# Kernel tuning notes

Measured on AMD Instinct MI355X. Metric: run time of the kernel, lower is better.

The kernel has to match this reference:

```python
import jax, jax.numpy as jnp
import numpy as np


def setup_inputs() -> dict:
    key = jax.random.key(0)
    ks = jax.random.split(key, 9)
    B, C, H, W = 4, 256, 128, 128
    d = C // 8
    x = jax.random.normal(ks[0], (B, C, H, W), jnp.float32)
    wq = jax.random.normal(ks[1], (d, C), jnp.float32) * 0.05
    bq = jax.random.normal(ks[2], (d,), jnp.float32) * 0.05
    wk = jax.random.normal(ks[3], (d, C), jnp.float32) * 0.05
    bk = jax.random.normal(ks[4], (d,), jnp.float32) * 0.05
    wv = jax.random.normal(ks[5], (d, C), jnp.float32) * 0.05
    bv = jax.random.normal(ks[6], (d,), jnp.float32) * 0.05
    wp = jax.random.normal(ks[7], (C, d, 3, 3), jnp.float32) * 0.05
    gamma = jax.random.normal(ks[8], (1,), jnp.float32)
    return dict(x=x, wq=wq, bq=bq, wk=wk, bk=bk, wv=wv, bv=bv, wp=wp, gamma=gamma)


def reference(x, wq, bq, wk, bk, wv, bv, wp, gamma):
    B, C, H, W = x.shape
    d = wq.shape[0]  # C // 8
    N = H * W
    # 1x1 convs expressed as channel matmuls
    q = jnp.einsum('bchw,dc->bdhw', x, wq) + bq[None, :, None, None]
    k = jnp.einsum('bchw,dc->bdhw', x, wk) + bk[None, :, None, None]
    v = jnp.einsum('bchw,dc->bdhw', x, wv) + bv[None, :, None, None]
    Q = q.reshape(B, d, N)
    K = k.reshape(B, d, N)
    V = v.reshape(B, d, N)
    # channel-channel energy: [B, d, d]
    energy = jnp.einsum('bdn,ben->bde', Q, K)
    energy_new = jnp.max(energy, axis=-1, keepdims=True) - energy
    attention = jax.nn.softmax(energy_new, axis=-1)
    out = jnp.einsum('bde,ben->bdn', attention, V).reshape(B, d, H, W)
    # 3x3 conv (no bias) + exact GELU
    out = jax.lax.conv_general_dilated(
        out, wp, window_strides=(1, 1), padding='SAME',
        dimension_numbers=('NCHW', 'OIHW', 'NCHW'))
    out = jax.nn.gelu(out, approximate=False)
    return gamma[0] * out + x
```

## Files before the change

### kernel.cpp

```cpp
#include <hip/hip_runtime.h>
#include <hip/hip_bf16.h>
#include <math.h>

#define BB 4
#define CC 256
#define HH 128
#define WW 128
#define NN (HH*WW)
#define DD 32

#define AOT_CI   44
#define AOT_ROWE (130*AOT_CI)
#define AOT_IMGE (130*AOT_ROWE)
#define AOT_BYTES ((size_t)BB*AOT_IMGE*2)
#define AOT_ALLOC (AOT_BYTES + 1024)

#define WT_BYTES (9*256*AOT_CI*2)

#define PATCH_SZ 45760
#define WSLAB    22528
#define CONV_LDS (PATCH_SZ + 2*WSLAB)
#define EPI_PITCH 260

#define ASWZ_BYTES 98304
#define QKP 260

typedef __attribute__((ext_vector_type(8)))  short bf16x8;
typedef __attribute__((ext_vector_type(4)))  float f32x4;
typedef __attribute__((ext_vector_type(16))) float f32x16;

__device__ inline void async_copy16(void* lds, const void* g) {
    __builtin_amdgcn_global_load_lds(
        (const __attribute__((address_space(1))) unsigned int*)g,
        (__attribute__((address_space(3))) unsigned int*)lds, 16, 0, 0);
}

__device__ inline unsigned short f2bf(float f) {
    __hip_bfloat16 h = __float2bfloat16(f);
    return *reinterpret_cast<unsigned short*>(&h);
}

__device__ inline void split2(float v, unsigned short& h, unsigned short& l) {
    __hip_bfloat16 hb = __float2bfloat16(v);
    float r = v - __bfloat162float(hb);
    __hip_bfloat16 lb = __float2bfloat16(r);
    h = *reinterpret_cast<unsigned short*>(&hb);
    l = *reinterpret_cast<unsigned short*>(&lb);
}

__device__ inline bf16x8 ld_frag8(const char* p) {
    union { bf16x8 v; short4 h[2]; } u;
    u.h[0] = *(const short4*)(p);
    u.h[1] = *(const short4*)(p + 8);
    return u.v;
}

__device__ inline float gelu_fast(float v) {
    float a = fabsf(v) * 0.70710678118654752f;
    float t = __fdividef(1.0f, fmaf(0.3275911f, a, 1.0f));
    float p = t * fmaf(t, fmaf(t, fmaf(t, fmaf(t, 1.061405429f, -1.453152027f),
                                       1.421413741f), -0.284496736f), 0.254829592f);
    float e = 1.0f - p * __expf(-a * a);
    float erfv = (v < 0.0f) ? -e : e;
    return 0.5f * v * (1.0f + erfv);
}

__global__ __launch_bounds__(256) void zero_kernel(uint4* __restrict__ p, int n16)
{
    for (int i = blockIdx.x*256 + threadIdx.x; i < n16; i += gridDim.x*256)
        p[i] = (uint4){0u, 0u, 0u, 0u};
}

__global__ __launch_bounds__(256) void wrepack2_kernel(
    const float* __restrict__ wq, const float* __restrict__ wk,
    const float* __restrict__ wv, unsigned short* __restrict__ Aswz)
{
    int i = blockIdx.x*256 + threadIdx.x;
    if (i >= 49152) return;
    int j    = i & 7;
    int lane = (i >> 3) & 63;
    int cf   = (i >> 9) % 3;
    int s    = i / 1536;
    int row  = cf*32 + (lane & 31);
    int k    = s*16 + (lane >> 5)*8 + j;
    int c    = k >> 1;
    float w  = (row < 32) ? wq[row*256 + c]
             : (row < 64) ? wk[(row-32)*256 + c]
                          : wv[(row-64)*256 + c];
    unsigned short h, l;
    split2(w, h, l);
    Aswz[i] = (k & 1) ? l : h;
}

__global__ __launch_bounds__(512, 1) void qkv_mfma_kernel(
    const float* __restrict__ x, const unsigned short* __restrict__ Aswz,
    const float* __restrict__ bq, const float* __restrict__ bk,
    const float* __restrict__ bv,
    float* __restrict__ Vout, float* __restrict__ Ep)
{
    __shared__ __align__(16) char lds[ASWZ_BYTES];
    __shared__ float biasL[96];
    const int b    = blockIdx.y;
    const int s    = blockIdx.x;
    const int n0   = s * 256;
    const int tid  = threadIdx.x;
    const int lane = tid & 63;
    const int wid  = tid >> 6;
    const int l31  = lane & 31;
    const int lh   = lane >> 5;
    const int nloc = 32*wid + l31;

    for (int i = tid; i < 6144; i += 512)
        async_copy16(lds + i*16, (const char*)Aswz + i*16);
    if (tid < 96)
        biasL[tid] = (tid < 32) ? bq[tid] : (tid < 64) ? bk[tid-32] : bv[tid-64];

    const float* xlane = x + ((size_t)b*CC + 4*lh)*NN + (n0 + nloc);

    f32x16 acc0 = {0}, acc1 = {0}, acc2 = {0};

    float xq[4][4];
    #pragma unroll
    for (int p0 = 0; p0 < 4; ++p0) {
        const float* p = xlane + (size_t)(8*p0)*NN;
        xq[p0][0] = p[0];            xq[p0][1] = p[(size_t)NN];
        xq[p0][2] = p[(size_t)2*NN]; xq[p0][3] = p[(size_t)3*NN];
    }

    __syncthreads();

    for (int su = 0; su < 32; su += 4) {
        #pragma unroll
        for (int ph = 0; ph < 4; ++ph) {
            const int st = su + ph;
            const char* ab = lds + (size_t)(st*3)*1024 + lane*16;
            bf16x8 a0 = *(const bf16x8*)(ab);
            bf16x8 a1 = *(const bf16x8*)(ab + 1024);
            bf16x8 a2 = *(const bf16x8*)(ab + 2048);
            float xv0 = xq[ph][0], xv1 = xq[ph][1];
            float xv2 = xq[ph][2], xv3 = xq[ph][3];
            if (st + 4 < 32) {
                const float* p = xlane + (size_t)(8*(st+4))*NN;
                xq[ph][0] = p[0];            xq[ph][1] = p[(size_t)NN];
                xq[ph][2] = p[(size_t)2*NN]; xq[ph][3] = p[(size_t)3*NN];
            }
            union { bf16x8 v; unsigned short u[8]; } B1, B2;
            unsigned short h, l;
            split2(xv0, h, l); B1.u[0] = h; B1.u[1] = h; B2.u[0] = l; B2.u[1] = l;
            split2(xv1, h, l); B1.u[2] = h; B1.u[3] = h; B2.u[2] = l; B2.u[3] = l;
            split2(xv2, h, l); B1.u[4] = h; B1.u[5] = h; B2.u[4] = l; B2.u[5] = l;
            split2(xv3, h, l); B1.u[6] = h; B1.u[7] = h; B2.u[6] = l; B2.u[7] = l;

            acc0 = __builtin_amdgcn_mfma_f32_32x32x16_bf16(a0, B1.v, acc0, 0, 0, 0);
            acc1 = __builtin_amdgcn_mfma_f32_32x32x16_bf16(a1, B1.v, acc1, 0, 0, 0);
            acc2 = __builtin_amdgcn_mfma_f32_32x32x16_bf16(a2, B1.v, acc2, 0, 0, 0);
            acc0 = __builtin_amdgcn_mfma_f32_32x32x16_bf16(a0, B2.v, acc0, 0, 0, 0);
            acc1 = __builtin_amdgcn_mfma_f32_32x32x16_bf16(a1, B2.v, acc1, 0, 0, 0);
            acc2 = __builtin_amdgcn_mfma_f32_32x32x16_bf16(a2, B2.v, acc2, 0, 0, 0);
        }
    }

    __syncthreads();
    float* qk = (float*)lds;
    #pragma unroll
    for (int r = 0; r < 16; ++r) {
        const int rsub = (r & 3) + 8*(r >> 2) + 4*lh;
        {
            const int row = rsub;
            qk[row*QKP + nloc] = acc0[r] + biasL[row];
        }
        {
            const int row = 32 + rsub;
            qk[row*QKP + nloc] = acc1[r] + biasL[row];
        }
        {
            const int row = 64 + rsub;
            Vout[((size_t)b*DD + rsub)*NN + n0 + nloc] = acc2[r] + biasL[row];
        }
    }
    __syncthreads();

    const int d  = tid >> 4;
    const int e0 = tid & 15;
    const float* qrow = qk + d*QKP;
    const float* ka   = qk + (32 + e0)*QKP;
    const float* kb   = qk + (48 + e0)*QKP;
    float s0 = 0.f, s1 = 0.f;
    for (int n4 = 0; n4 < 256; n4 += 4) {
        float4 qv = *(const float4*)(qrow + n4);
        float4 va = *(const float4*)(ka + n4);
        float4 vb = *(const float4*)(kb + n4);
        s0 += qv.x*va.x + qv.y*va.y + qv.z*va.z + qv.w*va.w;
        s1 += qv.x*vb.x + qv.y*vb.y + qv.z*vb.z + qv.w*vb.w;
    }
    float* ep = Ep + ((size_t)s*BB + b)*1024;
    ep[d*32 + e0]      = s0;
    ep[d*32 + e0 + 16] = s1;
}

__global__ __launch_bounds__(1024) void softmax_kernel(
    const float* __restrict__ Ep, float* __restrict__ attT)
{
    const int b = blockIdx.x;
    const int e = threadIdx.x, d = threadIdx.y;
    float s = 0.f;
    for (int p = 0; p < 64; ++p)
        s += Ep[((size_t)p * BB + b) * (DD * DD) + d * DD + e];
    float nv = -s;
    float m = nv;
    for (int off = 16; off > 0; off >>= 1) m = fmaxf(m, __shfl_xor(m, off, 32));
    float pe = expf(nv - m);
    float su = pe;
    for (int off = 16; off > 0; off >>= 1) su += __shfl_xor(su, off, 32);
    attT[(size_t)b * (DD * DD) + e * DD + d] = pe / su;
}

__global__ __launch_bounds__(256) void pv_kernel(
    const float* __restrict__ V, const float* __restrict__ attT,
    unsigned short* __restrict__ AOT)
{
    __shared__ float Vs[DD][256];
    __shared__ float at4[DD][DD];
    const int b  = blockIdx.y;
    const int n0 = blockIdx.x * 256;
    for (int i = threadIdx.x; i < DD * 256; i += 256) {
        int r = i >> 8, cc = i & 255;
        Vs[r][cc] = V[((size_t)b*DD + r)*NN + n0 + cc];
    }
    for (int i = threadIdx.x; i < DD * DD; i += 256)
        at4[i >> 5][i & 31] = attT[(size_t)b * (DD * DD) + i];
    __syncthreads();
    const int t = threadIdx.x;
    float acc[DD];
    #pragma unroll
    for (int d = 0; d < DD; ++d) acc[d] = 0.f;
    #pragma unroll 4
    for (int e = 0; e < DD; ++e) {
        float v = Vs[e][t];
        const float4* ar = (const float4*)at4[e];
        #pragma unroll
        for (int dq = 0; dq < 8; ++dq) {
            float4 a = ar[dq];
            acc[4*dq+0] += a.x * v; acc[4*dq+1] += a.y * v;
            acc[4*dq+2] += a.z * v; acc[4*dq+3] += a.w * v;
        }
    }
    const int n = n0 + t;
    const int h = n >> 7, w = n & 127;
    unsigned short* dst = AOT + (size_t)b*AOT_IMGE + (size_t)(h+1)*AOT_ROWE
                              + (size_t)(w+1)*AOT_CI;
    #pragma unroll
    for (int dq = 0; dq < 8; ++dq) {
        ushort4 u;
        u.x = f2bf(acc[4*dq+0]); u.y = f2bf(acc[4*dq+1]);
        u.z = f2bf(acc[4*dq+2]); u.w = f2bf(acc[4*dq+3]);
        *(ushort4*)(dst + 4*dq) = u;
    }
}

__global__ __launch_bounds__(256) void wrepack_kernel(
    const float* __restrict__ wp, unsigned short* __restrict__ Wt)
{
    int i = blockIdx.x * 256 + threadIdx.x;
    if (i >= 9*256*32) return;
    int kk = i / (256*32);
    int r  = i % (256*32);
    int co = r >> 5, ci = r & 31;
    float v = wp[((size_t)co*32 + ci)*9 + kk];
    Wt[((size_t)kk*256 + co)*AOT_CI + ci] = f2bf(v);
}

__global__ __launch_bounds__(512, 1) void conv_kernel(
    const unsigned short* __restrict__ AOT, const unsigned short* __restrict__ Wt,
    const float* __restrict__ gammap, const float* __restrict__ x,
    float* __restrict__ out)
{
    __shared__ __align__(16) char lds[CONV_LDS];
    const int b   = blockIdx.y;
    const int h0  = blockIdx.x * 2;
    const int tid = threadIdx.x;
    const int wid = tid >> 6;
    const int lane = tid & 63;
    const int l15 = lane & 15;
    const int lj  = lane >> 4;
    const int wn  = wid & 1;
    const int wc  = wid >> 1;

    const char* psrc = (const char*)(AOT + (size_t)b*AOT_IMGE + (size_t)h0*AOT_ROWE);
    for (int i = tid; i < PATCH_SZ/16; i += 512)
        async_copy16(lds + i*16, psrc + i*16);
    for (int i = tid; i < WSLAB/16; i += 512)
        async_copy16(lds + PATCH_SZ + i*16, (const char*)Wt + i*16);
    __syncthreads();

    f32x4 acc[4][8];
    #pragma unroll
    for (int cf = 0; cf < 4; ++cf)
        #pragma unroll
        for (int nf = 0; nf < 8; ++nf)
            acc[cf][nf] = (f32x4){0.f, 0.f, 0.f, 0.f};

    for (int kk = 0; kk < 9; ++kk) {
        if (kk < 8) {
            const char* wsrc = (const char*)Wt + (size_t)(kk+1)*WSLAB;
            char* wdst = lds + PATCH_SZ + ((kk+1)&1)*WSLAB;
            for (int i = tid; i < WSLAB/16; i += 512)
                async_copy16(wdst + i*16, wsrc + i*16);
        }
        const int kh = kk / 3, kw = kk % 3;
        const char* wbase = lds + PATCH_SZ + (kk&1)*WSLAB;
        bf16x8 af[4];
        #pragma unroll
        for (int cf = 0; cf < 4; ++cf)
            af[cf] = ld_frag8(wbase + (wc*64 + cf*16 + l15)*88 + lj*16);
        #pragma unroll
        for (int nf = 0; nf < 8; ++nf) {
            const int cell = (wn + kh)*130 + nf*16 + l15 + kw;
            const bf16x8 bfr = ld_frag8(lds + cell*88 + lj*16);
            #pragma unroll
            for (int cf = 0; cf < 4; ++cf)
                acc[cf][nf] = __builtin_amdgcn_mfma_f32_16x16x32_bf16(
                    af[cf], bfr, acc[cf][nf], 0, 0, 0);
        }
        __syncthreads();
    }

    const float g0 = gammap[0];
    float* lf = (float*)lds;
    for (int k = 0; k < 4; ++k) {
        if (wc == k) {
            #pragma unroll
            for (int cf = 0; cf < 4; ++cf) {
                const int rl = cf*16 + 4*lj;
                #pragma unroll
                for (int nf = 0; nf < 8; ++nf) {
                    const int col = wn*128 + nf*16 + l15;
                    #pragma unroll
                    for (int j = 0; j < 4; ++j)
                        lf[(rl + j)*EPI_PITCH + col] = acc[cf][nf][j];
                }
            }
        }
        __syncthreads();
        #pragma unroll
        for (int it = 0; it < 8; ++it) {
            const int idx = tid + it*512;
            const int row = idx >> 6, c4 = idx & 63;
            const int co  = k*64 + row;
            const size_t g = ((size_t)b*CC + co)*NN + (size_t)h0*WW + c4*4;
            float4 v  = *(const float4*)(lf + row*EPI_PITCH + c4*4);
            float4 xv = *(const float4*)(x + g);
            float4 o;
            o.x = g0*gelu_fast(v.x) + xv.x;
            o.y = g0*gelu_fast(v.y) + xv.y;
            o.z = g0*gelu_fast(v.z) + xv.z;
            o.w = g0*gelu_fast(v.w) + xv.w;
            *(float4*)(out + g) = o;
        }
        __syncthreads();
    }
}

extern "C" void kernel_launch(void* const* d_in, const int* in_sizes, int n_in,
                              void* d_out, int out_size, void* d_ws, size_t ws_size,
                              hipStream_t stream)
{
    const float* x  = (const float*)d_in[0];
    const float* wq = (const float*)d_in[1];
    const float* bq = (const float*)d_in[2];
    const float* wk = (const float*)d_in[3];
    const float* bk = (const float*)d_in[4];
    const float* wv = (const float*)d_in[5];
    const float* bv = (const float*)d_in[6];
    const float* wp = (const float*)d_in[7];
    const float* gm = (const float*)d_in[8];
    float* out = (float*)d_out;

    float* Vbuf = out;

    char* ws = (char*)d_ws;
    unsigned short* AOT  = (unsigned short*)ws;
    unsigned short* Wt   = (unsigned short*)(ws + AOT_ALLOC);
    unsigned short* Aswz = (unsigned short*)(ws + AOT_ALLOC + WT_BYTES);
    float* Ep  = (float*)(ws + AOT_ALLOC + WT_BYTES + ASWZ_BYTES);
    float* ATT = Ep + 64*BB*1024;

    zero_kernel    <<<dim3(1024), 256, 0, stream>>>((uint4*)AOT, (int)(AOT_ALLOC/16));
    wrepack_kernel <<<dim3(288), 256, 0, stream>>>(wp, Wt);
    wrepack2_kernel<<<dim3(192), 256, 0, stream>>>(wq, wk, wv, Aswz);
    qkv_mfma_kernel<<<dim3(64, BB), 512, 0, stream>>>(x, Aswz, bq, bk, bv, Vbuf, Ep);
    softmax_kernel <<<dim3(BB), dim3(32, 32), 0, stream>>>(Ep, ATT);
    pv_kernel      <<<dim3(NN/256, BB), 256, 0, stream>>>(Vbuf, ATT, AOT);
    conv_kernel    <<<dim3(64, BB), 512, 0, stream>>>(AOT, Wt, gm, x, out);
}
```

Before: 84.39 us.

## Merge prep kernels, zero only AOT borders, halve QKV tiles for higher occupancy

Folds the zero, conv-weight repack and QKV-weight repack kernels into one prep launch, and zeroes only the padding border of the AOT buffer instead of the whole allocation. The QKV kernel now uses 256-thread blocks over 128 columns with the weight slab staged in two halves, which halves its LDS footprint so several blocks can share a CU. The hi/lo split uses bit masking, and the pv kernel uses smaller tiles with vectorized V loads. The cost is twice as many partial energy tiles for softmax to reduce, plus an extra barrier and reload of the weight slab in every QKV block.

```diff
diff --git a/kernel.cpp b/kernel.cpp
--- a/kernel.cpp
+++ b/kernel.cpp
@@ -23,7 +23,8 @@
 #define EPI_PITCH 260
 
 #define ASWZ_BYTES 98304
-#define QKP 260
+#define AHALF      49152
+#define QK2        132
 
 typedef __attribute__((ext_vector_type(8)))  short bf16x8;
 typedef __attribute__((ext_vector_type(4)))  float f32x4;
@@ -65,44 +66,70 @@
     return 0.5f * v * (1.0f + erfv);
 }
 
-__global__ __launch_bounds__(256) void zero_kernel(uint4* __restrict__ p, int n16)
-{
-    for (int i = blockIdx.x*256 + threadIdx.x; i < n16; i += gridDim.x*256)
-        p[i] = (uint4){0u, 0u, 0u, 0u};
-}
-
-__global__ __launch_bounds__(256) void wrepack2_kernel(
+__global__ __launch_bounds__(256) void prep_kernel(
+    const float* __restrict__ wp, unsigned short* __restrict__ Wt,
     const float* __restrict__ wq, const float* __restrict__ wk,
-    const float* __restrict__ wv, unsigned short* __restrict__ Aswz)
-{
-    int i = blockIdx.x*256 + threadIdx.x;
-    if (i >= 49152) return;
-    int j    = i & 7;
-    int lane = (i >> 3) & 63;
-    int cf   = (i >> 9) % 3;
-    int s    = i / 1536;
-    int row  = cf*32 + (lane & 31);
-    int k    = s*16 + (lane >> 5)*8 + j;
-    int c    = k >> 1;
-    float w  = (row < 32) ? wq[row*256 + c]
-             : (row < 64) ? wk[(row-32)*256 + c]
-                          : wv[(row-64)*256 + c];
-    unsigned short h, l;
-    split2(w, h, l);
-    Aswz[i] = (k & 1) ? l : h;
-}
-
-__global__ __launch_bounds__(512, 1) void qkv_mfma_kernel(
+    const float* __restrict__ wv, unsigned short* __restrict__ Aswz,
+    unsigned short* __restrict__ AOT)
+{
+    const int blk = blockIdx.x;
+    if (blk < 288) {
+        int i = blk*256 + threadIdx.x;
+        int kk = i / (256*32);
+        int r  = i % (256*32);
+        int co = r >> 5, ci = r & 31;
+        float v = wp[((size_t)co*32 + ci)*9 + kk];
+        Wt[((size_t)kk*256 + co)*AOT_CI + ci] = f2bf(v);
+    } else if (blk < 480) {
+        int i = (blk-288)*256 + threadIdx.x;
+        int j    = i & 7;
+        int lane = (i >> 3) & 63;
+        int cf   = (i >> 9) % 3;
+        int s    = i / 1536;
+        int row  = cf*32 + (lane & 31);
+        int k    = s*16 + (lane >> 5)*8 + j;
+        int c    = k >> 1;
+        float w  = (row < 32) ? wq[row*256 + c]
+                 : (row < 64) ? wk[(row-32)*256 + c]
+                              : wv[(row-64)*256 + c];
+        unsigned short h, l;
+        split2(w, h, l);
+        Aswz[i] = (k & 1) ? l : h;
+    } else {
+        int idx = (blk-480)*256 + threadIdx.x;
+        if (idx < BB*22704) {
+            int b = idx / 22704;
+            int r = idx % 22704;
+            size_t off;
+            if (r < 11440) {
+                int row = (r < 5720) ? 0 : 129;
+                int e   = (r < 5720) ? r : r - 5720;
+                off = (size_t)b*AOT_IMGE + (size_t)row*AOT_ROWE + e;
+            } else {
+                int r2 = r - 11440;
+                int rr = r2 / 88 + 1;
+                int w2 = r2 % 88;
+                int col = (w2 < 44) ? 0 : 129;
+                int ci  = (w2 < 44) ? w2 : w2 - 44;
+                off = (size_t)b*AOT_IMGE + (size_t)rr*AOT_ROWE
+                    + (size_t)col*AOT_CI + ci;
+            }
+            AOT[off] = 0;
+        }
+    }
+}
+
+__global__ __launch_bounds__(256, 4) void qkv_mfma_kernel(
     const float* __restrict__ x, const unsigned short* __restrict__ Aswz,
     const float* __restrict__ bq, const float* __restrict__ bk,
     const float* __restrict__ bv,
     float* __restrict__ Vout, float* __restrict__ Ep)
 {
-    __shared__ __align__(16) char lds[ASWZ_BYTES];
+    __shared__ __align__(16) char lds[AHALF];
     __shared__ float biasL[96];
     const int b    = blockIdx.y;
     const int s    = blockIdx.x;
-    const int n0   = s * 256;
+    const int n0   = s * 128;
     const int tid  = threadIdx.x;
     const int lane = tid & 63;
     const int wid  = tid >> 6;
@@ -110,7 +137,7 @@
     const int lh   = lane >> 5;
     const int nloc = 32*wid + l31;
 
-    for (int i = tid; i < 6144; i += 512)
+    for (int i = tid; i < 3072; i += 256)
         async_copy16(lds + i*16, (const char*)Aswz + i*16);
     if (tid < 96)
         biasL[tid] = (tid < 32) ? bq[tid] : (tid < 64) ? bk[tid-32] : bv[tid-64];
@@ -127,75 +154,82 @@
         xq[p0][2] = p[(size_t)2*NN]; xq[p0][3] = p[(size_t)3*NN];
     }
 
-    __syncthreads();
-
-    for (int su = 0; su < 32; su += 4) {
-        #pragma unroll
-        for (int ph = 0; ph < 4; ++ph) {
-            const int st = su + ph;
-            const char* ab = lds + (size_t)(st*3)*1024 + lane*16;
-            bf16x8 a0 = *(const bf16x8*)(ab);
-            bf16x8 a1 = *(const bf16x8*)(ab + 1024);
-            bf16x8 a2 = *(const bf16x8*)(ab + 2048);
-            float xv0 = xq[ph][0], xv1 = xq[ph][1];
-            float xv2 = xq[ph][2], xv3 = xq[ph][3];
-            if (st + 4 < 32) {
-                const float* p = xlane + (size_t)(8*(st+4))*NN;
-                xq[ph][0] = p[0];            xq[ph][1] = p[(size_t)NN];
-                xq[ph][2] = p[(size_t)2*NN]; xq[ph][3] = p[(size_t)3*NN];
+    auto run_half = [&](int st_base) {
+        for (int su = 0; su < 16; su += 4) {
+            #pragma unroll
+            for (int ph = 0; ph < 4; ++ph) {
+                const int stl = su + ph;
+                const int st  = st_base + stl;
+                const char* ab = lds + (size_t)(stl*3)*1024 + lane*16;
+                bf16x8 a0 = *(const bf16x8*)(ab);
+                bf16x8 a1 = *(const bf16x8*)(ab + 1024);
+                bf16x8 a2 = *(const bf16x8*)(ab + 2048);
+                float v0 = xq[ph][0], v1 = xq[ph][1];
+                float v2 = xq[ph][2], v3 = xq[ph][3];
+                if (st + 4 < 32) {
+                    const float* p = xlane + (size_t)(8*(st+4))*NN;
+                    xq[ph][0] = p[0];            xq[ph][1] = p[(size_t)NN];
+                    xq[ph][2] = p[(size_t)2*NN]; xq[ph][3] = p[(size_t)3*NN];
+                }
+                union { bf16x8 v; unsigned int u[4]; } B1, B2;
+                #pragma unroll
+                for (int j = 0; j < 4; ++j) {
+                    float vj = (j==0)?v0:(j==1)?v1:(j==2)?v2:v3;
+                    unsigned int hb = __float_as_uint(vj) & 0xFFFF0000u;
+                    float rj = vj - __uint_as_float(hb);
+                    unsigned int lb = __float_as_uint(rj) >> 16;
+                    B1.u[j] = hb | (hb >> 16);
+                    B2.u[j] = lb | (lb << 16);
+                }
+                acc0 = __builtin_amdgcn_mfma_f32_32x32x16_bf16(a0, B1.v, acc0, 0, 0, 0);
+                acc1 = __builtin_amdgcn_mfma_f32_32x32x16_bf16(a1, B1.v, acc1, 0, 0, 0);
+                acc2 = __builtin_amdgcn_mfma_f32_32x32x16_bf16(a2, B1.v, acc2, 0, 0, 0);
+                acc0 = __builtin_amdgcn_mfma_f32_32x32x16_bf16(a0, B2.v, acc0, 0, 0, 0);
+                acc1 = __builtin_amdgcn_mfma_f32_32x32x16_bf16(a1, B2.v, acc1, 0, 0, 0);
+                acc2 = __builtin_amdgcn_mfma_f32_32x32x16_bf16(a2, B2.v, acc2, 0, 0, 0);
             }
-            union { bf16x8 v; unsigned short u[8]; } B1, B2;
-            unsigned short h, l;
-            split2(xv0, h, l); B1.u[0] = h; B1.u[1] = h; B2.u[0] = l; B2.u[1] = l;
-            split2(xv1, h, l); B1.u[2] = h; B1.u[3] = h; B2.u[2] = l; B2.u[3] = l;
-            split2(xv2, h, l); B1.u[4] = h; B1.u[5] = h; B2.u[4] = l; B2.u[5] = l;
-            split2(xv3, h, l); B1.u[6] = h; B1.u[7] = h; B2.u[6] = l; B2.u[7] = l;
-
-            acc0 = __builtin_amdgcn_mfma_f32_32x32x16_bf16(a0, B1.v, acc0, 0, 0, 0);
-            acc1 = __builtin_amdgcn_mfma_f32_32x32x16_bf16(a1, B1.v, acc1, 0, 0, 0);
-            acc2 = __builtin_amdgcn_mfma_f32_32x32x16_bf16(a2, B1.v, acc2, 0, 0, 0);
-            acc0 = __builtin_amdgcn_mfma_f32_32x32x16_bf16(a0, B2.v, acc0, 0, 0, 0);
-            acc1 = __builtin_amdgcn_mfma_f32_32x32x16_bf16(a1, B2.v, acc1, 0, 0, 0);
-            acc2 = __builtin_amdgcn_mfma_f32_32x32x16_bf16(a2, B2.v, acc2, 0, 0, 0);
-        }
-    }
+        }
+    };
+
+    __syncthreads();
+    run_half(0);
+    __syncthreads();
+    for (int i = tid; i < 3072; i += 256)
+        async_copy16(lds + i*16, (const char*)Aswz + AHALF + i*16);
+    __syncthreads();
+    run_half(16);
 
     __syncthreads();
     float* qk = (float*)lds;
     #pragma unroll
     for (int r = 0; r < 16; ++r) {
         const int rsub = (r & 3) + 8*(r >> 2) + 4*lh;
-        {
-            const int row = rsub;
-            qk[row*QKP + nloc] = acc0[r] + biasL[row];
-        }
-        {
-            const int row = 32 + rsub;
-            qk[row*QKP + nloc] = acc1[r] + biasL[row];
-        }
-        {
-            const int row = 64 + rsub;
-            Vout[((size_t)b*DD + rsub)*NN + n0 + nloc] = acc2[r] + biasL[row];
-        }
-    }
-    __syncthreads();
-
-    const int d  = tid >> 4;
-    const int e0 = tid & 15;
-    const float* qrow = qk + d*QKP;
-    const float* ka   = qk + (32 + e0)*QKP;
-    const float* kb   = qk + (48 + e0)*QKP;
-    float s0 = 0.f, s1 = 0.f;
-    for (int n4 = 0; n4 < 256; n4 += 4) {
+        qk[rsub*QK2 + nloc]      = acc0[r] + biasL[rsub];
+        qk[(32+rsub)*QK2 + nloc] = acc1[r] + biasL[32+rsub];
+        Vout[((size_t)b*DD + rsub)*NN + n0 + nloc] = acc2[r] + biasL[64+rsub];
+    }
+    __syncthreads();
+
+    const int d  = tid >> 3;
+    const int e0 = tid & 7;
+    const float* qrow = qk + d*QK2;
+    float s0 = 0.f, s1 = 0.f, s2 = 0.f, s3 = 0.f;
+    for (int n4 = 0; n4 < 128; n4 += 4) {
         float4 qv = *(const float4*)(qrow + n4);
-        float4 va = *(const float4*)(ka + n4);
-        float4 vb = *(const float4*)(kb + n4);
-        s0 += qv.x*va.x + qv.y*va.y + qv.z*va.z + qv.w*va.w;
-        s1 += qv.x*vb.x + qv.y*vb.y + qv.z*vb.z + qv.w*vb.w;
+        float4 k0 = *(const float4*)(qk + (32 + e0     )*QK2 + n4);
+        float4 k1 = *(const float4*)(qk + (32 + e0 +  8)*QK2 + n4);
+        float4 k2 = *(const float4*)(qk + (32 + e0 + 16)*QK2 + n4);
+        float4 k3 = *(const float4*)(qk + (32 + e0 + 24)*QK2 + n4);
+        s0 += qv.x*k0.x + qv.y*k0.y + qv.z*k0.z + qv.w*k0.w;
+        s1 += qv.x*k1.x + qv.y*k1.y + qv.z*k1.z + qv.w*k1.w;
+        s2 += qv.x*k2.x + qv.y*k2.y + qv.z*k2.z + qv.w*k2.w;
+        s3 += qv.x*k3.x + qv.y*k3.y + qv.z*k3.z + qv.w*k3.w;
     }
     float* ep = Ep + ((size_t)s*BB + b)*1024;
     ep[d*32 + e0]      = s0;
-    ep[d*32 + e0 + 16] = s1;
+    ep[d*32 + e0 + 8]  = s1;
+    ep[d*32 + e0 + 16] = s2;
+    ep[d*32 + e0 + 24] = s3;
 }
 
 __global__ __launch_bounds__(1024) void softmax_kernel(
@@ -204,7 +238,7 @@
     const int b = blockIdx.x;
     const int e = threadIdx.x, d = threadIdx.y;
     float s = 0.f;
-    for (int p = 0; p < 64; ++p)
+    for (int p = 0; p < 128; ++p)
         s += Ep[((size_t)p * BB + b) * (DD * DD) + d * DD + e];
     float nv = -s;
     float m = nv;
@@ -219,55 +253,46 @@
     const float* __restrict__ V, const float* __restrict__ attT,
     unsigned short* __restrict__ AOT)
 {
-    __shared__ float Vs[DD][256];
+    __shared__ float Vs[DD][128];
     __shared__ float at4[DD][DD];
     const int b  = blockIdx.y;
-    const int n0 = blockIdx.x * 256;
-    for (int i = threadIdx.x; i < DD * 256; i += 256) {
-        int r = i >> 8, cc = i & 255;
-        Vs[r][cc] = V[((size_t)b*DD + r)*NN + n0 + cc];
-    }
-    for (int i = threadIdx.x; i < DD * DD; i += 256)
-        at4[i >> 5][i & 31] = attT[(size_t)b * (DD * DD) + i];
-    __syncthreads();
-    const int t = threadIdx.x;
-    float acc[DD];
+    const int n0 = blockIdx.x * 128;
+    const int tid = threadIdx.x;
+    for (int i = tid; i < 1024; i += 256) {
+        int r = i >> 5, c4 = i & 31;
+        *(float4*)&Vs[r][c4*4] =
+            *(const float4*)(V + ((size_t)b*DD + r)*NN + n0 + c4*4);
+    }
+    for (int i = tid; i < 1024; i += 256)
+        at4[i >> 5][i & 31] = attT[(size_t)b*1024 + i];
+    __syncthreads();
+    const int nl = tid & 127;
+    const int dg = tid >> 7;
+    float acc[16];
     #pragma unroll
-    for (int d = 0; d < DD; ++d) acc[d] = 0.f;
+    for (int k = 0; k < 16; ++k) acc[k] = 0.f;
     #pragma unroll 4
     for (int e = 0; e < DD; ++e) {
-        float v = Vs[e][t];
-        const float4* ar = (const float4*)at4[e];
+        float v = Vs[e][nl];
+        const float4* ar = (const float4*)&at4[e][dg*16];
         #pragma unroll
-        for (int dq = 0; dq < 8; ++dq) {
-            float4 a = ar[dq];
-            acc[4*dq+0] += a.x * v; acc[4*dq+1] += a.y * v;
-            acc[4*dq+2] += a.z * v; acc[4*dq+3] += a.w * v;
-        }
-    }
-    const int n = n0 + t;
+        for (int q = 0; q < 4; ++q) {
+            float4 a = ar[q];
+            acc[4*q+0] += a.x * v; acc[4*q+1] += a.y * v;
+            acc[4*q+2] += a.z * v; acc[4*q+3] += a.w * v;
+        }
+    }
+    const int n = n0 + nl;
     const int h = n >> 7, w = n & 127;
     unsigned short* dst = AOT + (size_t)b*AOT_IMGE + (size_t)(h+1)*AOT_ROWE
-                              + (size_t)(w+1)*AOT_CI;
+                              + (size_t)(w+1)*AOT_CI + dg*16;
     #pragma unroll
-    for (int dq = 0; dq < 8; ++dq) {
+    for (int q = 0; q < 4; ++q) {
         ushort4 u;
-        u.x = f2bf(acc[4*dq+0]); u.y = f2bf(acc[4*dq+1]);
-        u.z = f2bf(acc[4*dq+2]); u.w = f2bf(acc[4*dq+3]);
-        *(ushort4*)(dst + 4*dq) = u;
-    }
-}
-
-__global__ __launch_bounds__(256) void wrepack_kernel(
-    const float* __restrict__ wp, unsigned short* __restrict__ Wt)
-{
-    int i = blockIdx.x * 256 + threadIdx.x;
-    if (i >= 9*256*32) return;
-    int kk = i / (256*32);
-    int r  = i % (256*32);
-    int co = r >> 5, ci = r & 31;
-    float v = wp[((size_t)co*32 + ci)*9 + kk];
-    Wt[((size_t)kk*256 + co)*AOT_CI + ci] = f2bf(v);
+        u.x = f2bf(acc[4*q+0]); u.y = f2bf(acc[4*q+1]);
+        u.z = f2bf(acc[4*q+2]); u.w = f2bf(acc[4*q+3]);
+        *(ushort4*)(dst + 4*q) = u;
+    }
 }
 
 __global__ __launch_bounds__(512, 1) void conv_kernel(
@@ -383,13 +408,11 @@
     unsigned short* Wt   = (unsigned short*)(ws + AOT_ALLOC);
     unsigned short* Aswz = (unsigned short*)(ws + AOT_ALLOC + WT_BYTES);
     float* Ep  = (float*)(ws + AOT_ALLOC + WT_BYTES + ASWZ_BYTES);
-    float* ATT = Ep + 64*BB*1024;
-
-    zero_kernel    <<<dim3(1024), 256, 0, stream>>>((uint4*)AOT, (int)(AOT_ALLOC/16));
-    wrepack_kernel <<<dim3(288), 256, 0, stream>>>(wp, Wt);
-    wrepack2_kernel<<<dim3(192), 256, 0, stream>>>(wq, wk, wv, Aswz);
-    qkv_mfma_kernel<<<dim3(64, BB), 512, 0, stream>>>(x, Aswz, bq, bk, bv, Vbuf, Ep);
+    float* ATT = Ep + (size_t)128*BB*1024;
+
+    prep_kernel    <<<dim3(1024), 256, 0, stream>>>(wp, Wt, wq, wk, wv, Aswz, AOT);
+    qkv_mfma_kernel<<<dim3(128, BB), 256, 0, stream>>>(x, Aswz, bq, bk, bv, Vbuf, Ep);
     softmax_kernel <<<dim3(BB), dim3(32, 32), 0, stream>>>(Ep, ATT);
-    pv_kernel      <<<dim3(NN/256, BB), 256, 0, stream>>>(Vbuf, ATT, AOT);
+    pv_kernel      <<<dim3(128, BB), 256, 0, stream>>>(Vbuf, ATT, AOT);
     conv_kernel    <<<dim3(64, BB), 512, 0, stream>>>(AOT, Wt, gm, x, out);
 }
```

After: 85.89 us. No clear change (+1.8%).
